# Optimization experiments

Hardware: AMD Instinct MI355X
Metric: run time of the kernel (lower is better)

The kernel has to match this reference:

```python
import jax, jax.numpy as jnp
from jax import lax
import numpy as np

N, C, H, W = 8, 64, 256, 256


def setup_inputs() -> dict:
    key = jax.random.key(0)
    k1, k2, k3, k4 = jax.random.split(key, 4)
    X = jax.random.normal(k1, (N, C, H, W), dtype=jnp.float32)
    # gates in [0, 1/3) so g1+g2+g3 < 1 -> stable propagation (SPN normalizes gates)
    G1 = jax.random.uniform(k2, (N, C, H, W), dtype=jnp.float32) / 3.0
    G2 = jax.random.uniform(k3, (N, C, H, W), dtype=jnp.float32) / 3.0
    G3 = jax.random.uniform(k4, (N, C, H, W), dtype=jnp.float32) / 3.0
    return {"X": X, "G1": G1, "G2": G2, "G3": G3}


def _spn_scan(X, G1, G2, G3):
    # horizontal=True, reverse=False: left-to-right scan over W.
    # Put scan axis (W) first; per-step slabs are [N, C, H].
    xs = tuple(jnp.moveaxis(a, 3, 0) for a in (X, G1, G2, G3))

    def step(h_prev, ins):
        x, g1, g2, g3 = ins  # each [N, C, H]
        zero = jnp.zeros_like(h_prev[..., :1])
        h_up = jnp.concatenate([zero, h_prev[..., :-1]], axis=-1)    # h_prev[i-1]
        h_dn = jnp.concatenate([h_prev[..., 1:], zero], axis=-1)     # h_prev[i+1]
        h = x * (1.0 - g1 - g2 - g3) + g1 * h_up + g2 * h_prev + g3 * h_dn
        return h, h

    h0 = jnp.zeros(xs[0].shape[1:], X.dtype)
    _, hs = lax.scan(step, h0, xs)  # hs: [W, N, C, H]
    return jnp.moveaxis(hs, 0, 3)   # [N, C, H, W]


def reference(X, G1, G2, G3):
    return _spn_scan(X, G1, G2, G3)
```

## Files before the change

kernel.cpp:

```cpp
#include <hip/hip_runtime.h>


constexpr int Hh  = 256;
constexpr int Ww  = 256;
constexpr int WT  = 16;
constexpr int PAD = WT + 1;

__global__ __launch_bounds__(256, 2)
void spn_scan_kernel(const float* __restrict__ X,
                     const float* __restrict__ G1,
                     const float* __restrict__ G2,
                     const float* __restrict__ G3,
                     float* __restrict__ O)
{
    __shared__ float xt [Hh * PAD];
    __shared__ float g1t[Hh * PAD];
    __shared__ float g2t[Hh * PAD];
    __shared__ float g3t[Hh * PAD];
    __shared__ float hbuf[2][Hh + 2];

    const int t     = threadIdx.x;
    const int plane = blockIdx.x;
    const int base  = plane * (Hh * Ww);

    if (t < 2) {
        hbuf[t][0]      = 0.0f;
        hbuf[t][Hh + 1] = 0.0f;
    }

    float h = 0.0f;

    const int lrow = t >> 2;
    const int lcol = (t & 3) << 2;

    for (int w0 = 0; w0 < Ww; w0 += WT) {
        __syncthreads();

        #pragma unroll
        for (int q = 0; q < 4; ++q) {
            const int row = q * 64 + lrow;
            const int g   = base + row * Ww + w0 + lcol;
            const int l   = row * PAD + lcol;
            const float4 vx = *reinterpret_cast<const float4*>(X  + g);
            const float4 v1 = *reinterpret_cast<const float4*>(G1 + g);
            const float4 v2 = *reinterpret_cast<const float4*>(G2 + g);
            const float4 v3 = *reinterpret_cast<const float4*>(G3 + g);
            xt [l+0]=vx.x; xt [l+1]=vx.y; xt [l+2]=vx.z; xt [l+3]=vx.w;
            g1t[l+0]=v1.x; g1t[l+1]=v1.y; g1t[l+2]=v1.z; g1t[l+3]=v1.w;
            g2t[l+0]=v2.x; g2t[l+1]=v2.y; g2t[l+2]=v2.z; g2t[l+3]=v2.w;
            g3t[l+0]=v3.x; g3t[l+1]=v3.y; g3t[l+2]=v3.z; g3t[l+3]=v3.w;
        }
        __syncthreads();

        #pragma unroll
        for (int ww = 0; ww < WT; ++ww) {
            float* hb = hbuf[ww & 1];
            hb[t + 1] = h;
            __syncthreads();
            const float hu = hb[t];
            const float hd = hb[t + 2];
            const int   l  = t * PAD + ww;
            const float x  = xt [l];
            const float g1 = g1t[l];
            const float g2 = g2t[l];
            const float g3 = g3t[l];
            const float a  = 1.0f - g1 - g2 - g3;
            h = fmaf(g3, hd, fmaf(g2, h, fmaf(g1, hu, x * a)));
            xt[l] = h;
        }
        __syncthreads();

        #pragma unroll
        for (int q = 0; q < 4; ++q) {
            const int row = q * 64 + lrow;
            const int l   = row * PAD + lcol;
            const float4 v = make_float4(xt[l+0], xt[l+1], xt[l+2], xt[l+3]);
            const int g   = base + row * Ww + w0 + lcol;
            *reinterpret_cast<float4*>(O + g) = v;
        }
    }
}

extern "C" void kernel_launch(void* const* d_in, const int* in_sizes, int n_in,
                              void* d_out, int out_size, void* d_ws, size_t ws_size,
                              hipStream_t stream) {
    const float* X  = (const float*)d_in[0];
    const float* G1 = (const float*)d_in[1];
    const float* G2 = (const float*)d_in[2];
    const float* G3 = (const float*)d_in[3];
    float* O = (float*)d_out;

    const int planes = 8 * 64;
    spn_scan_kernel<<<dim3(planes), dim3(256), 0, stream>>>(X, G1, G2, G3, O);
}
```

Baseline: 193.1 us.

## Move SPN scan to single-wavefront register tiles with shuffle neighbor exchange

Replaces the 256-thread block, which staged tiles in shared memory and synchronised at every column step, with one 64-lane wavefront per plane. Each lane owns 4 consecutive rows, exchanges boundary values with neighbouring lanes via shuffles, and double-buffers 4-column tiles in registers. This removes LDS traffic and per-step barriers. The cost is only 64 threads per block, which lowers memory-level parallelism, and strided float4 loads per lane that coalesce less well than before.

```diff
diff --git a/kernel.cpp b/kernel.cpp
--- a/kernel.cpp
+++ b/kernel.cpp
@@ -1,82 +1,109 @@
 #include <hip/hip_runtime.h>
 
 
-constexpr int Hh  = 256;
-constexpr int Ww  = 256;
-constexpr int WT  = 16;
-constexpr int PAD = WT + 1;
+constexpr int H  = 256;
+constexpr int W  = 256;
+constexpr int WT = 4;
+constexpr int NT = W / WT;
 
-__global__ __launch_bounds__(256, 2)
-void spn_scan_kernel(const float* __restrict__ X,
-                     const float* __restrict__ G1,
-                     const float* __restrict__ G2,
-                     const float* __restrict__ G3,
-                     float* __restrict__ O)
+struct Tile {
+    float4 x[4], g1[4], g2[4], g3[4];
+};
+
+__device__ __forceinline__
+void load_tile(Tile& t, const float* __restrict__ px, const float* __restrict__ p1,
+               const float* __restrict__ p2, const float* __restrict__ p3, int w)
 {
-    __shared__ float xt [Hh * PAD];
-    __shared__ float g1t[Hh * PAD];
-    __shared__ float g2t[Hh * PAD];
-    __shared__ float g3t[Hh * PAD];
-    __shared__ float hbuf[2][Hh + 2];
+#pragma unroll
+    for (int r = 0; r < 4; ++r) {
+        t.x [r] = *reinterpret_cast<const float4*>(px + r * W + w);
+        t.g1[r] = *reinterpret_cast<const float4*>(p1 + r * W + w);
+        t.g2[r] = *reinterpret_cast<const float4*>(p2 + r * W + w);
+        t.g3[r] = *reinterpret_cast<const float4*>(p3 + r * W + w);
+    }
+}
 
-    const int t     = threadIdx.x;
-    const int plane = blockIdx.x;
-    const int base  = plane * (Hh * Ww);
+__device__ __forceinline__
+void compute_tile(const Tile& t, float h[4], float4 o[4], int lane)
+{
+#pragma unroll
+    for (int c = 0; c < 4; ++c) {
+        float up = __shfl_up (h[3], 1);
+        float dn = __shfl_down(h[0], 1);
+        up = (lane == 0)  ? 0.0f : up;
+        dn = (lane == 63) ? 0.0f : dn;
+        float n0, n1, n2, n3;
+        {
+            const float x  = (&t.x [0].x)[c], g1 = (&t.g1[0].x)[c];
+            const float g2 = (&t.g2[0].x)[c], g3 = (&t.g3[0].x)[c];
+            const float a  = 1.0f - g1 - g2 - g3;
+            n0 = fmaf(g3, h[1], fmaf(g2, h[0], fmaf(g1, up,   x * a)));
+        }
+        {
+            const float x  = (&t.x [1].x)[c], g1 = (&t.g1[1].x)[c];
+            const float g2 = (&t.g2[1].x)[c], g3 = (&t.g3[1].x)[c];
+            const float a  = 1.0f - g1 - g2 - g3;
+            n1 = fmaf(g3, h[2], fmaf(g2, h[1], fmaf(g1, h[0], x * a)));
+        }
+        {
+            const float x  = (&t.x [2].x)[c], g1 = (&t.g1[2].x)[c];
+            const float g2 = (&t.g2[2].x)[c], g3 = (&t.g3[2].x)[c];
+            const float a  = 1.0f - g1 - g2 - g3;
+            n2 = fmaf(g3, h[3], fmaf(g2, h[2], fmaf(g1, h[1], x * a)));
+        }
+        {
+            const float x  = (&t.x [3].x)[c], g1 = (&t.g1[3].x)[c];
+            const float g2 = (&t.g2[3].x)[c], g3 = (&t.g3[3].x)[c];
+            const float a  = 1.0f - g1 - g2 - g3;
+            n3 = fmaf(g3, dn,   fmaf(g2, h[3], fmaf(g1, h[2], x * a)));
+        }
+        h[0] = n0; h[1] = n1; h[2] = n2; h[3] = n3;
+        (&o[0].x)[c] = n0; (&o[1].x)[c] = n1; (&o[2].x)[c] = n2; (&o[3].x)[c] = n3;
+    }
+}
 
-    if (t < 2) {
-        hbuf[t][0]      = 0.0f;
-        hbuf[t][Hh + 1] = 0.0f;
-    }
+__device__ __forceinline__
+void store_tile(float* __restrict__ po, const float4 o[4], int w)
+{
+#pragma unroll
+    for (int r = 0; r < 4; ++r)
+        *reinterpret_cast<float4*>(po + r * W + w) = o[r];
+}
 
-    float h = 0.0f;
+__global__ __launch_bounds__(64)
+void spn_scan_regs(const float* __restrict__ X,  const float* __restrict__ G1,
+                   const float* __restrict__ G2, const float* __restrict__ G3,
+                   float* __restrict__ O)
+{
+    const int lane = threadIdx.x;
+    const size_t base = (size_t)blockIdx.x * (H * W) + (size_t)(lane * 4) * W;
+    const float* px = X  + base;
+    const float* p1 = G1 + base;
+    const float* p2 = G2 + base;
+    const float* p3 = G3 + base;
+    float*       po = O  + base;
 
-    const int lrow = t >> 2;
-    const int lcol = (t & 3) << 2;
+    float  h[4] = {0.0f, 0.0f, 0.0f, 0.0f};
+    float4 o[4];
+    Tile A, B;
 
-    for (int w0 = 0; w0 < Ww; w0 += WT) {
-        __syncthreads();
+    load_tile(A, px, p1, p2, p3, 0);
+    load_tile(B, px, p1, p2, p3, WT);
 
-        #pragma unroll
-        for (int q = 0; q < 4; ++q) {
-            const int row = q * 64 + lrow;
-            const int g   = base + row * Ww + w0 + lcol;
-            const int l   = row * PAD + lcol;
-            const float4 vx = *reinterpret_cast<const float4*>(X  + g);
-            const float4 v1 = *reinterpret_cast<const float4*>(G1 + g);
-            const float4 v2 = *reinterpret_cast<const float4*>(G2 + g);
-            const float4 v3 = *reinterpret_cast<const float4*>(G3 + g);
-            xt [l+0]=vx.x; xt [l+1]=vx.y; xt [l+2]=vx.z; xt [l+3]=vx.w;
-            g1t[l+0]=v1.x; g1t[l+1]=v1.y; g1t[l+2]=v1.z; g1t[l+3]=v1.w;
-            g2t[l+0]=v2.x; g2t[l+1]=v2.y; g2t[l+2]=v2.z; g2t[l+3]=v2.w;
-            g3t[l+0]=v3.x; g3t[l+1]=v3.y; g3t[l+2]=v3.z; g3t[l+3]=v3.w;
+    for (int t0 = 0; t0 < NT; t0 += 2) {
+        compute_tile(A, h, o, lane);
+        store_tile(po, o, t0 * WT);
+        {
+            int wn = (t0 + 2) * WT;
+            if (wn > W - WT) wn = W - WT;
+            load_tile(A, px, p1, p2, p3, wn);
         }
-        __syncthreads();
-
-        #pragma unroll
-        for (int ww = 0; ww < WT; ++ww) {
-            float* hb = hbuf[ww & 1];
-            hb[t + 1] = h;
-            __syncthreads();
-            const float hu = hb[t];
-            const float hd = hb[t + 2];
-            const int   l  = t * PAD + ww;
-            const float x  = xt [l];
-            const float g1 = g1t[l];
-            const float g2 = g2t[l];
-            const float g3 = g3t[l];
-            const float a  = 1.0f - g1 - g2 - g3;
-            h = fmaf(g3, hd, fmaf(g2, h, fmaf(g1, hu, x * a)));
-            xt[l] = h;
-        }
-        __syncthreads();
-
-        #pragma unroll
-        for (int q = 0; q < 4; ++q) {
-            const int row = q * 64 + lrow;
-            const int l   = row * PAD + lcol;
-            const float4 v = make_float4(xt[l+0], xt[l+1], xt[l+2], xt[l+3]);
-            const int g   = base + row * Ww + w0 + lcol;
-            *reinterpret_cast<float4*>(O + g) = v;
+        compute_tile(B, h, o, lane);
+        store_tile(po, o, (t0 + 1) * WT);
+        {
+            int wn = (t0 + 3) * WT;
+            if (wn > W - WT) wn = W - WT;
+            load_tile(B, px, p1, p2, p3, wn);
         }
     }
 }
@@ -91,5 +118,5 @@
     float* O = (float*)d_out;
 
     const int planes = 8 * 64;
-    spn_scan_kernel<<<dim3(planes), dim3(256), 0, stream>>>(X, G1, G2, G3, O);
+    spn_scan_regs<<<dim3(planes), dim3(64), 0, stream>>>(X, G1, G2, G3, O);
 }
```

New measurement: 554.3 us. 187% more time.

## Run each plane's scan in one wavefront with shuffles and async LDS prefetch

Applied to the files above, without the earlier changes.

Replaces the 256-thread block, which needed a __syncthreads on every column step to exchange neighbour rows, with a single 64-lane wave per plane. Each lane owns four consecutive rows, so neighbour values come from registers and cross-lane shuffles instead of shared-memory barriers. Input tiles eight columns wide are streamed into a double-buffered LDS area with global_load_lds and explicit vmcnt waits, so the loads for the next tiles overlap the serial recurrence. Outputs are kept in registers and written as float4 every sixteen columns. The trade-off is only one wave per plane, 512 waves in total, so occupancy is low and memory bandwidth must come from the deep prefetch rather than from many resident waves.

```diff
diff --git a/kernel.cpp b/kernel.cpp
--- a/kernel.cpp
+++ b/kernel.cpp
@@ -1,82 +1,124 @@
 #include <hip/hip_runtime.h>
+#include <cstdint>
 
 
-constexpr int Hh  = 256;
-constexpr int Ww  = 256;
-constexpr int WT  = 16;
-constexpr int PAD = WT + 1;
+constexpr int H  = 256;
+constexpr int W  = 256;
+constexpr int WT = 8;
+constexpr int NT = W / WT;
 
-__global__ __launch_bounds__(256, 2)
-void spn_scan_kernel(const float* __restrict__ X,
-                     const float* __restrict__ G1,
-                     const float* __restrict__ G2,
-                     const float* __restrict__ G3,
-                     float* __restrict__ O)
+#define F4C(v, j) ((&(v).x)[j])
+
+typedef const __attribute__((address_space(1))) void* gas_ptr;
+typedef __attribute__((address_space(3))) void* las_ptr;
+
+__device__ __forceinline__ void gload_lds16(const float* g, float4* l) {
+    __builtin_amdgcn_global_load_lds((gas_ptr)(const void*)g, (las_ptr)(void*)l,
+                                     16, 0, 0);
+}
+
+__global__ __launch_bounds__(64)
+void spn_wave(const float* __restrict__ X,  const float* __restrict__ G1,
+              const float* __restrict__ G2, const float* __restrict__ G3,
+              float* __restrict__ O)
 {
-    __shared__ float xt [Hh * PAD];
-    __shared__ float g1t[Hh * PAD];
-    __shared__ float g2t[Hh * PAD];
-    __shared__ float g3t[Hh * PAD];
-    __shared__ float hbuf[2][Hh + 2];
+    __shared__ float4 lds[2][4][2][4][64];
 
-    const int t     = threadIdx.x;
-    const int plane = blockIdx.x;
-    const int base  = plane * (Hh * Ww);
+    const int    l  = threadIdx.x;
+    const size_t pb = (size_t)blockIdx.x * (H * W);
+    const float* __restrict__ in0 = X  + pb;
+    const float* __restrict__ in1 = G1 + pb;
+    const float* __restrict__ in2 = G2 + pb;
+    const float* __restrict__ in3 = G3 + pb;
+    float* __restrict__ out = O + pb;
 
-    if (t < 2) {
-        hbuf[t][0]      = 0.0f;
-        hbuf[t][Hh + 1] = 0.0f;
-    }
+    auto issue = [&](int t, int b) {
+        const int w = t * WT;
+#pragma unroll
+        for (int s = 0; s < 2; ++s)
+#pragma unroll
+            for (int r = 0; r < 4; ++r) {
+                const int goff = (4 * l + r) * W + w + 4 * s;
+                gload_lds16(in0 + goff, &lds[b][0][s][r][0]);
+                gload_lds16(in1 + goff, &lds[b][1][s][r][0]);
+                gload_lds16(in2 + goff, &lds[b][2][s][r][0]);
+                gload_lds16(in3 + goff, &lds[b][3][s][r][0]);
+            }
+    };
 
-    float h = 0.0f;
+    issue(0, 0);
+    issue(1, 1);
 
-    const int lrow = t >> 2;
-    const int lcol = (t & 3) << 2;
+    float h0 = 0.f, h1 = 0.f, h2 = 0.f, h3 = 0.f;
+    float4 o[4][4];
 
-    for (int w0 = 0; w0 < Ww; w0 += WT) {
-        __syncthreads();
+    for (int p = 0; p < NT / 2; ++p) {
+#pragma unroll
+        for (int half = 0; half < 2; ++half) {
+            const int  t       = 2 * p + half;
+            const int  b       = half;
+            const bool steady  = (t + 2 < NT);
 
-        #pragma unroll
-        for (int q = 0; q < 4; ++q) {
-            const int row = q * 64 + lrow;
-            const int g   = base + row * Ww + w0 + lcol;
-            const int l   = row * PAD + lcol;
-            const float4 vx = *reinterpret_cast<const float4*>(X  + g);
-            const float4 v1 = *reinterpret_cast<const float4*>(G1 + g);
-            const float4 v2 = *reinterpret_cast<const float4*>(G2 + g);
-            const float4 v3 = *reinterpret_cast<const float4*>(G3 + g);
-            xt [l+0]=vx.x; xt [l+1]=vx.y; xt [l+2]=vx.z; xt [l+3]=vx.w;
-            g1t[l+0]=v1.x; g1t[l+1]=v1.y; g1t[l+2]=v1.z; g1t[l+3]=v1.w;
-            g2t[l+0]=v2.x; g2t[l+1]=v2.y; g2t[l+2]=v2.z; g2t[l+3]=v2.w;
-            g3t[l+0]=v3.x; g3t[l+1]=v3.y; g3t[l+2]=v3.z; g3t[l+3]=v3.w;
+            if (steady) asm volatile("s_waitcnt vmcnt(32)" ::: "memory");
+            else        asm volatile("s_waitcnt vmcnt(0)"  ::: "memory");
+
+            float4 xr[4][2], a1[4][2], a2[4][2], a3[4][2];
+#pragma unroll
+            for (int s = 0; s < 2; ++s)
+#pragma unroll
+                for (int r = 0; r < 4; ++r) {
+                    xr[r][s] = lds[b][0][s][r][l];
+                    a1[r][s] = lds[b][1][s][r][l];
+                    a2[r][s] = lds[b][2][s][r][l];
+                    a3[r][s] = lds[b][3][s][r][l];
+                }
+            asm volatile("s_waitcnt lgkmcnt(0)" ::: "memory");
+            if (steady) issue(t + 2, b);
+
+#pragma unroll
+            for (int s = 0; s < 2; ++s)
+#pragma unroll
+                for (int j = 0; j < 4; ++j) {
+                    float up = __shfl_up(h3, 1);
+                    float dn = __shfl_down(h0, 1);
+                    if (l == 0)  up = 0.f;
+                    if (l == 63) dn = 0.f;
+
+                    const float x0 = F4C(xr[0][s], j), g10 = F4C(a1[0][s], j),
+                                g20 = F4C(a2[0][s], j), g30 = F4C(a3[0][s], j);
+                    const float x1 = F4C(xr[1][s], j), g11 = F4C(a1[1][s], j),
+                                g21 = F4C(a2[1][s], j), g31 = F4C(a3[1][s], j);
+                    const float x2 = F4C(xr[2][s], j), g12 = F4C(a1[2][s], j),
+                                g22 = F4C(a2[2][s], j), g32 = F4C(a3[2][s], j);
+                    const float x3 = F4C(xr[3][s], j), g13 = F4C(a1[3][s], j),
+                                g23 = F4C(a2[3][s], j), g33 = F4C(a3[3][s], j);
+
+                    const float n0 = fmaf(g30, h1, fmaf(g20, h0,
+                                     fmaf(g10, up, x0 * (1.f - g10 - g20 - g30))));
+                    const float n1 = fmaf(g31, h2, fmaf(g21, h1,
+                                     fmaf(g11, h0, x1 * (1.f - g11 - g21 - g31))));
+                    const float n2 = fmaf(g32, h3, fmaf(g22, h2,
+                                     fmaf(g12, h1, x2 * (1.f - g12 - g22 - g32))));
+                    const float n3 = fmaf(g33, dn, fmaf(g23, h3,
+                                     fmaf(g13, h2, x3 * (1.f - g13 - g23 - g33))));
+
+                    h0 = n0; h1 = n1; h2 = n2; h3 = n3;
+                    const int oc = half * 2 + s;
+                    F4C(o[0][oc], j) = n0;
+                    F4C(o[1][oc], j) = n1;
+                    F4C(o[2][oc], j) = n2;
+                    F4C(o[3][oc], j) = n3;
+                }
         }
-        __syncthreads();
 
-        #pragma unroll
-        for (int ww = 0; ww < WT; ++ww) {
-            float* hb = hbuf[ww & 1];
-            hb[t + 1] = h;
-            __syncthreads();
-            const float hu = hb[t];
-            const float hd = hb[t + 2];
-            const int   l  = t * PAD + ww;
-            const float x  = xt [l];
-            const float g1 = g1t[l];
-            const float g2 = g2t[l];
-            const float g3 = g3t[l];
-            const float a  = 1.0f - g1 - g2 - g3;
-            h = fmaf(g3, hd, fmaf(g2, h, fmaf(g1, hu, x * a)));
-            xt[l] = h;
-        }
-        __syncthreads();
-
-        #pragma unroll
-        for (int q = 0; q < 4; ++q) {
-            const int row = q * 64 + lrow;
-            const int l   = row * PAD + lcol;
-            const float4 v = make_float4(xt[l+0], xt[l+1], xt[l+2], xt[l+3]);
-            const int g   = base + row * Ww + w0 + lcol;
-            *reinterpret_cast<float4*>(O + g) = v;
+        const int wp = p * 16;
+#pragma unroll
+        for (int r = 0; r < 4; ++r) {
+            float* po = out + (4 * l + r) * W + wp;
+            *reinterpret_cast<float4*>(po)      = o[r][0];
+            *reinterpret_cast<float4*>(po + 4)  = o[r][1];
+            *reinterpret_cast<float4*>(po + 8)  = o[r][2];
+            *reinterpret_cast<float4*>(po + 12) = o[r][3];
         }
     }
 }
@@ -91,5 +133,5 @@
     float* O = (float*)d_out;
 
     const int planes = 8 * 64;
-    spn_scan_kernel<<<dim3(planes), dim3(256), 0, stream>>>(X, G1, G2, G3, O);
+    spn_wave<<<dim3(planes), dim3(64), 0, stream>>>(X, G1, G2, G3, O);
 }
```

After: 522.6 us. 2.71x slower.

## Double-buffer input tiles with register prefetch and write outputs directly from registers

Applied to the files above, without the earlier changes.

The scan now prefetches the next tiles of X and gates into registers while the current tile is computed, and stages them into a double-buffered shared-memory area. This overlaps global loads with the serial per-column recurrence. Tile width drops to 8 and each thread keeps its row's results in registers, writing them straight to global as float4 instead of going back through shared memory. The cost is more registers, the same 64KB of LDS, and per-thread row-wise stores that are strided across threads, which may hurt coalescing.

```diff
diff --git a/kernel.cpp b/kernel.cpp
--- a/kernel.cpp
+++ b/kernel.cpp
@@ -1,83 +1,103 @@
 #include <hip/hip_runtime.h>
 
 
-constexpr int Hh  = 256;
-constexpr int Ww  = 256;
-constexpr int WT  = 16;
-constexpr int PAD = WT + 1;
+constexpr int H    = 256;
+constexpr int W    = 256;
+constexpr int WT   = 8;
+constexpr int NT   = W / WT;
+constexpr int PADW = 9;
 
 __global__ __launch_bounds__(256, 2)
-void spn_scan_kernel(const float* __restrict__ X,
-                     const float* __restrict__ G1,
-                     const float* __restrict__ G2,
-                     const float* __restrict__ G3,
-                     float* __restrict__ O)
+void spn_block(const float* __restrict__ X,  const float* __restrict__ G1,
+               const float* __restrict__ G2, const float* __restrict__ G3,
+               float* __restrict__ O)
 {
-    __shared__ float xt [Hh * PAD];
-    __shared__ float g1t[Hh * PAD];
-    __shared__ float g2t[Hh * PAD];
-    __shared__ float g3t[Hh * PAD];
-    __shared__ float hbuf[2][Hh + 2];
+    __shared__ float sb[2][4][256 * PADW];
+    __shared__ float hb[2][258];
 
-    const int t     = threadIdx.x;
-    const int plane = blockIdx.x;
-    const int base  = plane * (Hh * Ww);
+    const int    t  = threadIdx.x;
+    const size_t pb = (size_t)blockIdx.x * (size_t)(H * W);
+    const float* __restrict__ a0 = X  + pb;
+    const float* __restrict__ a1 = G1 + pb;
+    const float* __restrict__ a2 = G2 + pb;
+    const float* __restrict__ a3 = G3 + pb;
 
-    if (t < 2) {
-        hbuf[t][0]      = 0.0f;
-        hbuf[t][Hh + 1] = 0.0f;
-    }
+    const int srow = t >> 1, scol = (t & 1) << 2;
+    float4 rg[4][2];
 
-    float h = 0.0f;
+    auto issue = [&](int tile) {
+        const int w0 = tile * WT + scol;
+#pragma unroll
+        for (int p = 0; p < 2; ++p) {
+            const size_t off = (size_t)(p * 128 + srow) * W + w0;
+            rg[0][p] = *reinterpret_cast<const float4*>(a0 + off);
+            rg[1][p] = *reinterpret_cast<const float4*>(a1 + off);
+            rg[2][p] = *reinterpret_cast<const float4*>(a2 + off);
+            rg[3][p] = *reinterpret_cast<const float4*>(a3 + off);
+        }
+    };
+    auto stage = [&](int b) {
+#pragma unroll
+        for (int p = 0; p < 2; ++p) {
+            const int l = (p * 128 + srow) * PADW + scol;
+#pragma unroll
+            for (int a = 0; a < 4; ++a) {
+                sb[b][a][l + 0] = (&rg[a][p].x)[0];
+                sb[b][a][l + 1] = (&rg[a][p].x)[1];
+                sb[b][a][l + 2] = (&rg[a][p].x)[2];
+                sb[b][a][l + 3] = (&rg[a][p].x)[3];
+            }
+        }
+    };
 
-    const int lrow = t >> 2;
-    const int lcol = (t & 3) << 2;
+    if (t < 2) { hb[0][t * 257] = 0.f; hb[1][t * 257] = 0.f; }
 
-    for (int w0 = 0; w0 < Ww; w0 += WT) {
+    issue(0); stage(0);
+    issue(1);
+    __syncthreads();
+
+    float h = 0.f;
+    const int lrow = t * PADW;
+
+    auto do_tile = [&](int tile, float (&o8)[8]) {
+        const float* __restrict__ xb = sb[tile & 1][0];
+        const float* __restrict__ b1 = sb[tile & 1][1];
+        const float* __restrict__ b2 = sb[tile & 1][2];
+        const float* __restrict__ b3 = sb[tile & 1][3];
+
+        float qx[8], q1[8], q2[8], q3[8];
+#pragma unroll
+        for (int ww = 0; ww < 8; ++ww) {
+            qx[ww] = xb[lrow + ww]; q1[ww] = b1[lrow + ww];
+            q2[ww] = b2[lrow + ww]; q3[ww] = b3[lrow + ww];
+        }
+#pragma unroll
+        for (int ww = 0; ww < 8; ++ww) {
+            float* hp = hb[ww & 1];
+            hp[t + 1] = h;
+            __syncthreads();
+            const float hu = hp[t], hd = hp[t + 2];
+            h = fmaf(q3[ww], hd, fmaf(q2[ww], h, fmaf(q1[ww], hu,
+                     qx[ww] * (1.f - q1[ww] - q2[ww] - q3[ww]))));
+            o8[ww] = h;
+        }
+        if (tile + 1 < NT) stage((tile + 1) & 1);
+        if (tile + 2 < NT) issue(tile + 2);
         __syncthreads();
+    };
 
-        #pragma unroll
-        for (int q = 0; q < 4; ++q) {
-            const int row = q * 64 + lrow;
-            const int g   = base + row * Ww + w0 + lcol;
-            const int l   = row * PAD + lcol;
-            const float4 vx = *reinterpret_cast<const float4*>(X  + g);
-            const float4 v1 = *reinterpret_cast<const float4*>(G1 + g);
-            const float4 v2 = *reinterpret_cast<const float4*>(G2 + g);
-            const float4 v3 = *reinterpret_cast<const float4*>(G3 + g);
-            xt [l+0]=vx.x; xt [l+1]=vx.y; xt [l+2]=vx.z; xt [l+3]=vx.w;
-            g1t[l+0]=v1.x; g1t[l+1]=v1.y; g1t[l+2]=v1.z; g1t[l+3]=v1.w;
-            g2t[l+0]=v2.x; g2t[l+1]=v2.y; g2t[l+2]=v2.z; g2t[l+3]=v2.w;
-            g3t[l+0]=v3.x; g3t[l+1]=v3.y; g3t[l+2]=v3.z; g3t[l+3]=v3.w;
-        }
-        __syncthreads();
+    float* __restrict__ orow = O + pb + (size_t)t * W;
 
-        #pragma unroll
-        for (int ww = 0; ww < WT; ++ww) {
-            float* hb = hbuf[ww & 1];
-            hb[t + 1] = h;
-            __syncthreads();
-            const float hu = hb[t];
-            const float hd = hb[t + 2];
-            const int   l  = t * PAD + ww;
-            const float x  = xt [l];
-            const float g1 = g1t[l];
-            const float g2 = g2t[l];
-            const float g3 = g3t[l];
-            const float a  = 1.0f - g1 - g2 - g3;
-            h = fmaf(g3, hd, fmaf(g2, h, fmaf(g1, hu, x * a)));
-            xt[l] = h;
-        }
-        __syncthreads();
-
-        #pragma unroll
-        for (int q = 0; q < 4; ++q) {
-            const int row = q * 64 + lrow;
-            const int l   = row * PAD + lcol;
-            const float4 v = make_float4(xt[l+0], xt[l+1], xt[l+2], xt[l+3]);
-            const int g   = base + row * Ww + w0 + lcol;
-            *reinterpret_cast<float4*>(O + g) = v;
-        }
+#pragma unroll 1
+    for (int p = 0; p < NT / 2; ++p) {
+        float oA[8], oB[8];
+        do_tile(2 * p,     oA);
+        do_tile(2 * p + 1, oB);
+        float* po = orow + p * 16;
+        *reinterpret_cast<float4*>(po +  0) = make_float4(oA[0], oA[1], oA[2], oA[3]);
+        *reinterpret_cast<float4*>(po +  4) = make_float4(oA[4], oA[5], oA[6], oA[7]);
+        *reinterpret_cast<float4*>(po +  8) = make_float4(oB[0], oB[1], oB[2], oB[3]);
+        *reinterpret_cast<float4*>(po + 12) = make_float4(oB[4], oB[5], oB[6], oB[7]);
     }
 }
 
@@ -91,5 +111,5 @@
     float* O = (float*)d_out;
 
     const int planes = 8 * 64;
-    spn_scan_kernel<<<dim3(planes), dim3(256), 0, stream>>>(X, G1, G2, G3, O);
+    spn_block<<<dim3(planes), dim3(256), 0, stream>>>(X, G1, G2, G3, O);
 }
```

After: 281.6 us. 1.46x slower.
